# Optimization experiments

Measured on AMD Instinct MI355X. Metric: run time of the kernel, lower is better.

## Reference

```python
import jax, jax.numpy as jnp
import numpy as np
import math
jax.config.update("jax_enable_x64", True)

# dims matching init_kwargs
BS, N_IND, N_STEP, ORDER = 32, 8, 100, 2
N_ORD = ORDER + 1            # number of derivative orders tracked (y, y', y'')
N_IV, N_IV_STEPS = 2, 1
NVAR = N_STEP * N_ORD        # qp variables per ODE (eps column is dropped: A[..., 1:])
DT = jnp.float64             # solver_dbl=True


def _static_parts():
    # initial-value constraint rows: u[t, j] = iv_rhs for t < n_iv_steps, j < n_iv
    iv_rows = N_IV_STEPS * N_IV
    Iv = np.zeros((iv_rows, NVAR))
    r = 0
    for t in range(N_IV_STEPS):
        for j in range(N_IV):
            Iv[r, t * N_ORD + j] = 1.0
            r += 1
    # Taylor expansion tables: fact[i, j] = 1/(j-i)! for j>=i else 0; expn[i,j] = j-i
    i_idx = np.arange(ORDER)[:, None]
    j_idx = np.arange(N_ORD)[None, :]
    dmask = j_idx >= i_idx
    d = np.where(dmask, j_idx - i_idx, 0)
    fact = np.where(dmask, 1.0 / np.array([[math.factorial(v) for v in row] for row in d]), 0.0)
    sign = np.where(dmask, (-1.0) ** d, 0.0)
    Imat = np.eye(ORDER, N_ORD)
    return (jnp.asarray(Iv, DT), jnp.asarray(fact, DT), jnp.asarray(d, DT),
            jnp.asarray(sign, DT), jnp.asarray(Imat, DT))


def _solve(coeffs, rhs, iv_rhs, steps):
    # coeffs: (B, n_step, n_ord), rhs: (B, n_step), iv_rhs: (B, iv_rows), steps: (B, n_step-1)
    B = coeffs.shape[0]
    T1 = N_STEP - 1
    R = 2 * ORDER + 1  # fwd Taylor rows (ORDER) + bwd Taylor rows (ORDER) + central row (1)
    Iv, fact, expn, sign, Imat = _static_parts()

    # equation constraints: block-diagonal in step: sum_j coeffs[b,t,j] * u[t,j] = rhs[b,t]
    eye = jnp.eye(N_STEP, dtype=DT)
    Eq = jnp.einsum('ts,bsj->btsj', eye, coeffs).reshape(B, N_STEP, NVAR)
    IvB = jnp.broadcast_to(Iv[None], (B,) + Iv.shape)

    # smoothness constraints per interval t -> t+1 with step h = steps[b,t]
    h = steps[:, :, None, None]                  # (B, T1, 1, 1)
    hp = h ** expn                               # h^(j-i)
    fwd_t = fact * hp                            # fwd Taylor: sum_j h^(j-i)/(j-i)! u[t,j] - u[t+1,i] = 0
    bwd_t1 = fact * sign * hp                    # bwd Taylor: sum_j (-h)^(j-i)/(j-i)! u[t+1,j] - u[t,i] = 0
    ImB = jnp.broadcast_to(Imat, fwd_t.shape)
    hh = steps[:, :, None]                       # (B, T1, 1)
    e_m1 = jnp.zeros((N_ORD,), DT).at[ORDER - 1].set(1.0)
    e_o = jnp.zeros((N_ORD,), DT).at[ORDER].set(1.0)
    # central (trapezoid) rule on highest derivative:
    # u[t+1,ord-1] - u[t,ord-1] - h/2 (u[t,ord] + u[t+1,ord]) = 0
    ct = -e_m1 - 0.5 * hh * e_o                  # (B, T1, n_ord) coeffs on block t
    ct1 = e_m1 - 0.5 * hh * e_o                  # coeffs on block t+1
    Dt = jnp.concatenate([fwd_t, -ImB, ct[:, :, None, :]], axis=2)    # (B,T1,R,n_ord)
    Dt1 = jnp.concatenate([-ImB, bwd_t1, ct1[:, :, None, :]], axis=2)

    Dfull = jnp.zeros((B, T1, R, N_STEP, N_ORD), DT)
    t = jnp.arange(T1)
    Dfull = Dfull.at[:, t, :, t, :].set(jnp.moveaxis(Dt, 1, 0))
    Dfull = Dfull.at[:, t, :, t + 1, :].set(jnp.moveaxis(Dt1, 1, 0))
    D = Dfull.reshape(B, T1 * R, NVAR)

    A = jnp.concatenate([Eq, IvB, D], axis=1)    # dense AG (eps column dropped)
    beta = jnp.concatenate([rhs, iv_rhs, jnp.zeros((B, T1 * R), DT)], axis=1)

    AtA = jnp.einsum('bmi,bmj->bij', A, A)
    Atb = jnp.einsum('bmi,bm->bi', A, beta)
    L = jnp.linalg.cholesky(AtA)
    x = jax.scipy.linalg.cho_solve((L, True), Atb[..., None])[..., 0]
    return x


def setup_inputs() -> dict:
    key = jax.random.key(0)
    k1, k2, k3, k4 = jax.random.split(key, 4)
    coeffs = jax.random.normal(k1, (BS, N_IND, N_STEP, N_ORD), dtype=jnp.float32)
    rhs = jax.random.normal(k2, (BS, N_IND, N_STEP), dtype=jnp.float32)
    iv_rhs = jax.random.normal(k3, (BS, N_IND, N_IV_STEPS * N_IV), dtype=jnp.float32)
    # positive step sizes around the module's step_size=0.1
    steps = 0.05 + 0.1 * jax.random.uniform(k4, (BS, N_IND, N_STEP - 1), dtype=jnp.float32)
    return {"coeffs": coeffs, "rhs": rhs, "iv_rhs": iv_rhs, "steps": steps}


def reference(coeffs, rhs, iv_rhs, steps):
    B = BS * N_IND
    c = coeffs.reshape(B, N_STEP, N_ORD).astype(DT)   # n_dim = 1 folded in
    r = rhs.reshape(B, N_STEP).astype(DT)
    iv = iv_rhs.reshape(B, N_IV_STEPS * N_IV).astype(DT)
    st = steps.reshape(B, N_STEP - 1).astype(DT)
    x = _solve(c, r, iv, st)
    u = x.reshape(BS, N_IND, N_STEP, N_ORD)
    u0, u1, u2 = u[..., 0], u[..., 1], u[..., 2]
    eps = jnp.zeros((B,), DT)
    return (u0, u1, u2, eps, st[:, :, None])
```

## Files before the change

kernel.cpp:

```cpp
#include <hip/hip_runtime.h>

#define NPROB 256
#define NSTEP 100
#define T1    99

__device__ __forceinline__ void syminv3(const double A[6], double G[6]) {
    const double k00 = A[3] * A[5] - A[4] * A[4];
    const double k01 = A[2] * A[4] - A[1] * A[5];
    const double k02 = A[1] * A[4] - A[2] * A[3];
    const double det = A[0] * k00 + A[1] * k01 + A[2] * k02;
    const double id  = 1.0 / det;
    G[0] = k00 * id;
    G[1] = k01 * id;
    G[2] = k02 * id;
    G[3] = (A[0] * A[5] - A[2] * A[2]) * id;
    G[4] = (A[2] * A[1] - A[0] * A[4]) * id;
    G[5] = (A[0] * A[3] - A[1] * A[1]) * id;
}

__device__ __forceinline__ void symmul(const double G[6], const double M[9], double R[9]) {
#pragma unroll
    for (int c = 0; c < 3; ++c) {
        R[0 + c] = G[0] * M[c] + G[1] * M[3 + c] + G[2] * M[6 + c];
        R[3 + c] = G[1] * M[c] + G[3] * M[3 + c] + G[4] * M[6 + c];
        R[6 + c] = G[2] * M[c] + G[4] * M[3 + c] + G[5] * M[6 + c];
    }
}

__device__ __forceinline__ void symvec(const double G[6], const double v[3], double r[3]) {
    r[0] = G[0] * v[0] + G[1] * v[1] + G[2] * v[2];
    r[1] = G[1] * v[0] + G[3] * v[1] + G[4] * v[2];
    r[2] = G[2] * v[0] + G[4] * v[1] + G[5] * v[2];
}

__device__ __forceinline__ void pqz(const double A[6], const double C[9],
                                    const double B[9], const double b[3],
                                    double P[9], double Q[9], double z[3]) {
    double G[6];
    syminv3(A, G);
    symmul(G, C, P);
    symmul(G, B, Q);
    symvec(G, b, z);
}

__device__ __forceinline__ void store21(double* dst, const double P[9],
                                        const double Q[9], const double z[3]) {
#pragma unroll
    for (int k = 0; k < 9; ++k) { dst[k] = P[k]; dst[9 + k] = Q[k]; }
#pragma unroll
    for (int k = 0; k < 3; ++k) dst[18 + k] = z[k];
}

__device__ __forceinline__ void upd(double A[6], double C[9], double B[9], double b[3],
                                    const double* SL, const double* SR) {
    double Pl[9], Ql[9], zl[3], Pr[9], Qr[9], zr[3];
#pragma unroll
    for (int k = 0; k < 9; ++k) { Pl[k] = SL[k]; Ql[k] = SL[9 + k]; }
#pragma unroll
    for (int k = 0; k < 3; ++k) zl[k] = SL[18 + k];
#pragma unroll
    for (int k = 0; k < 9; ++k) { Pr[k] = SR[k]; Qr[k] = SR[9 + k]; }
#pragma unroll
    for (int k = 0; k < 3; ++k) zr[k] = SR[18 + k];

    const int RI[6] = {0, 0, 0, 1, 1, 2};
    const int CI[6] = {0, 1, 2, 1, 2, 2};
#pragma unroll
    for (int e = 0; e < 6; ++e) {
        const int r = RI[e], c = CI[e];
        A[e] -= C[3 * r] * Ql[c] + C[3 * r + 1] * Ql[3 + c] + C[3 * r + 2] * Ql[6 + c]
              + B[3 * r] * Pr[c] + B[3 * r + 1] * Pr[3 + c] + B[3 * r + 2] * Pr[6 + c];
    }
    double nC[9], nB[9];
#pragma unroll
    for (int r = 0; r < 3; ++r)
#pragma unroll
        for (int c = 0; c < 3; ++c) {
            nC[3 * r + c] = -(C[3 * r] * Pl[c] + C[3 * r + 1] * Pl[3 + c] + C[3 * r + 2] * Pl[6 + c]);
            nB[3 * r + c] = -(B[3 * r] * Qr[c] + B[3 * r + 1] * Qr[3 + c] + B[3 * r + 2] * Qr[6 + c]);
        }
#pragma unroll
    for (int r = 0; r < 3; ++r)
        b[r] -= C[3 * r] * zl[0] + C[3 * r + 1] * zl[1] + C[3 * r + 2] * zl[2]
              + B[3 * r] * zr[0] + B[3 * r + 1] * zr[1] + B[3 * r + 2] * zr[2];
#pragma unroll
    for (int k = 0; k < 9; ++k) { C[k] = nC[k]; B[k] = nB[k]; }
}

__device__ __forceinline__ void build_row(int t, const float* cb, const float* rb,
                                          const float* sb, const float* ivp,
                                          double A[6], double C[9], double B[9], double b[3]) {
    const double c0 = (double)cb[t * 3 + 0];
    const double c1 = (double)cb[t * 3 + 1];
    const double c2 = (double)cb[t * 3 + 2];
    const double r  = (double)rb[t];
    A[0] = c0 * c0; A[1] = c0 * c1; A[2] = c0 * c2;
    A[3] = c1 * c1; A[4] = c1 * c2; A[5] = c2 * c2;
    b[0] = c0 * r;  b[1] = c1 * r;  b[2] = c2 * r;
#pragma unroll
    for (int k = 0; k < 9; ++k) { C[k] = 0.0; B[k] = 0.0; }

    if (t == 0) {
        A[0] += 1.0; A[3] += 1.0;
        b[0] += (double)ivp[0];
        b[1] += (double)ivp[1];
    }
    if (t < T1) {
        const double h = (double)sb[t], h2 = h * h;
        A[0] += 2.0;
        A[1] += h;
        A[2] += 0.5 * h2;
        A[3] += h2 + 3.0;
        A[4] += 0.5 * h2 * h + 1.5 * h;
        A[5] += 0.25 * h2 * h2 + 1.25 * h2;
        B[0] = -2.0;       B[1] =  h;         B[2] = -0.5 * h2;
        B[3] = -h;         B[4] = -3.0;       B[5] =  1.5 * h;
        B[6] = -0.5 * h2;  B[7] = -1.5 * h;   B[8] =  0.25 * h2;
    }
    if (t > 0) {
        const double hm = (double)sb[t - 1], hm2 = hm * hm;
        A[0] += 2.0;
        A[1] -= hm;
        A[2] += 0.5 * hm2;
        A[3] += hm2 + 3.0;
        A[4] -= 0.5 * hm2 * hm + 1.5 * hm;
        A[5] += 0.25 * hm2 * hm2 + 1.25 * hm2;
        C[0] = -2.0;       C[1] = -hm;        C[2] = -0.5 * hm2;
        C[3] =  hm;        C[4] = -3.0;       C[5] = -1.5 * hm;
        C[6] = -0.5 * hm2; C[7] =  1.5 * hm;  C[8] =  0.25 * hm2;
    }
}

__global__ __launch_bounds__(64, 1) void ode_pcr_kernel(
    const float* __restrict__ coeffs,
    const float* __restrict__ rhs,
    const float* __restrict__ iv_rhs,
    const float* __restrict__ steps,
    float* __restrict__ out)
{
    const int b = blockIdx.x;
    const int L = threadIdx.x;

    __shared__ double S[114][21];
    __shared__ double X[52][3];

    for (int i = L; i < 114 * 21; i += 64) ((double*)S)[i] = 0.0;
    for (int i = L; i < 52 * 3;  i += 64) ((double*)X)[i] = 0.0;

    const float* cb  = coeffs + b * NSTEP * 3;
    const float* rb  = rhs    + b * NSTEP;
    const float* sb  = steps  + b * T1;
    const float* ivp = iv_rhs + b * 2;

    const bool act = (L < 50);
    double Ae[6], Ce[9], Be[9], be[3];
    double Po[9], Qo[9], zo[3];

    __syncthreads();

    if (act) {
        build_row(2 * L, cb, rb, sb, ivp, Ae, Ce, Be, be);
        double Ao[6], Co[9], Bo[9], bo[3];
        build_row(2 * L + 1, cb, rb, sb, ivp, Ao, Co, Bo, bo);
        pqz(Ao, Co, Bo, bo, Po, Qo, zo);
        store21(&S[L + 32][0], Po, Qo, zo);
    }
    __syncthreads();
    if (act) upd(Ae, Ce, Be, be, &S[L + 31][0], &S[L + 32][0]);
    __syncthreads();

#pragma unroll
    for (int lv = 0; lv < 6; ++lv) {
        const int s = 1 << lv;
        if (act) {
            double P[9], Q[9], z[3];
            pqz(Ae, Ce, Be, be, P, Q, z);
            store21(&S[L + 32][0], P, Q, z);
        }
        __syncthreads();
        if (act) upd(Ae, Ce, Be, be, &S[L + 32 - s][0], &S[L + 32 + s][0]);
        __syncthreads();
    }

    double xe[3] = {0.0, 0.0, 0.0};
    if (act) {
        double G[6];
        syminv3(Ae, G);
        symvec(G, be, xe);
        X[L + 1][0] = xe[0]; X[L + 1][1] = xe[1]; X[L + 1][2] = xe[2];
    }
    __syncthreads();

    if (act) {
        const double xr0 = X[L + 2][0], xr1 = X[L + 2][1], xr2 = X[L + 2][2];
        double xo[3];
#pragma unroll
        for (int r = 0; r < 3; ++r)
            xo[r] = zo[r]
                  - (Po[3 * r] * xe[0] + Po[3 * r + 1] * xe[1] + Po[3 * r + 2] * xe[2])
                  - (Qo[3 * r] * xr0   + Qo[3 * r + 1] * xr1   + Qo[3 * r + 2] * xr2);

        const int t0 = 2 * L, t1 = 2 * L + 1;
        out[            b * NSTEP + t0] = (float)xe[0];
        out[            b * NSTEP + t1] = (float)xo[0];
        out[25600 +     b * NSTEP + t0] = (float)xe[1];
        out[25600 +     b * NSTEP + t1] = (float)xo[1];
        out[51200 +     b * NSTEP + t0] = (float)xe[2];
        out[51200 +     b * NSTEP + t1] = (float)xo[2];
    }

    for (int t = L; t < T1; t += 64)
        out[77056 + b * T1 + t] = sb[t];
    if (L == 0)
        out[76800 + b] = 0.0f;
}

extern "C" void kernel_launch(void* const* d_in, const int* in_sizes, int n_in,
                              void* d_out, int out_size, void* d_ws, size_t ws_size,
                              hipStream_t stream) {
    const float* coeffs = (const float*)d_in[0];
    const float* rhs    = (const float*)d_in[1];
    const float* iv_rhs = (const float*)d_in[2];
    const float* steps  = (const float*)d_in[3];
    float* out = (float*)d_out;

    ode_pcr_kernel<<<dim3(NPROB), dim3(64), 0, stream>>>(
        coeffs, rhs, iv_rhs, steps, out);
}
```

Baseline: 66.89 us.

## Switch PCR solver to fp32 and exchange neighbor blocks via wavefront shuffles

```diff
diff --git a/kernel.cpp b/kernel.cpp
--- a/kernel.cpp
+++ b/kernel.cpp
@@ -4,12 +4,12 @@
 #define NSTEP 100
 #define T1    99
 
-__device__ __forceinline__ void syminv3(const double A[6], double G[6]) {
-    const double k00 = A[3] * A[5] - A[4] * A[4];
-    const double k01 = A[2] * A[4] - A[1] * A[5];
-    const double k02 = A[1] * A[4] - A[2] * A[3];
-    const double det = A[0] * k00 + A[1] * k01 + A[2] * k02;
-    const double id  = 1.0 / det;
+__device__ __forceinline__ void syminv3(const float A[6], float G[6]) {
+    const float k00 = A[3] * A[5] - A[4] * A[4];
+    const float k01 = A[2] * A[4] - A[1] * A[5];
+    const float k02 = A[1] * A[4] - A[2] * A[3];
+    const float det = A[0] * k00 + A[1] * k01 + A[2] * k02;
+    const float id  = 1.0f / det;
     G[0] = k00 * id;
     G[1] = k01 * id;
     G[2] = k02 * id;
@@ -18,7 +18,7 @@
     G[5] = (A[0] * A[3] - A[1] * A[1]) * id;
 }
 
-__device__ __forceinline__ void symmul(const double G[6], const double M[9], double R[9]) {
+__device__ __forceinline__ void symmul(const float G[6], const float M[9], float R[9]) {
 #pragma unroll
     for (int c = 0; c < 3; ++c) {
         R[0 + c] = G[0] * M[c] + G[1] * M[3 + c] + G[2] * M[6 + c];
@@ -27,41 +27,25 @@
     }
 }
 
-__device__ __forceinline__ void symvec(const double G[6], const double v[3], double r[3]) {
+__device__ __forceinline__ void symvec(const float G[6], const float v[3], float r[3]) {
     r[0] = G[0] * v[0] + G[1] * v[1] + G[2] * v[2];
     r[1] = G[1] * v[0] + G[3] * v[1] + G[4] * v[2];
     r[2] = G[2] * v[0] + G[4] * v[1] + G[5] * v[2];
 }
 
-__device__ __forceinline__ void pqz(const double A[6], const double C[9],
-                                    const double B[9], const double b[3],
-                                    double P[9], double Q[9], double z[3]) {
-    double G[6];
+__device__ __forceinline__ void pqz(const float A[6], const float C[9],
+                                    const float B[9], const float b[3], float pub[21]) {
+    float G[6];
     syminv3(A, G);
-    symmul(G, C, P);
-    symmul(G, B, Q);
-    symvec(G, b, z);
-}
-
-__device__ __forceinline__ void store21(double* dst, const double P[9],
-                                        const double Q[9], const double z[3]) {
-#pragma unroll
-    for (int k = 0; k < 9; ++k) { dst[k] = P[k]; dst[9 + k] = Q[k]; }
-#pragma unroll
-    for (int k = 0; k < 3; ++k) dst[18 + k] = z[k];
-}
-
-__device__ __forceinline__ void upd(double A[6], double C[9], double B[9], double b[3],
-                                    const double* SL, const double* SR) {
-    double Pl[9], Ql[9], zl[3], Pr[9], Qr[9], zr[3];
-#pragma unroll
-    for (int k = 0; k < 9; ++k) { Pl[k] = SL[k]; Ql[k] = SL[9 + k]; }
-#pragma unroll
-    for (int k = 0; k < 3; ++k) zl[k] = SL[18 + k];
-#pragma unroll
-    for (int k = 0; k < 9; ++k) { Pr[k] = SR[k]; Qr[k] = SR[9 + k]; }
-#pragma unroll
-    for (int k = 0; k < 3; ++k) zr[k] = SR[18 + k];
+    symmul(G, C, pub);
+    symmul(G, B, pub + 9);
+    symvec(G, b, pub + 18);
+}
+
+__device__ __forceinline__ void upd(float A[6], float C[9], float B[9], float b[3],
+                                    const float SL[21], const float SR[21]) {
+    const float* Pl = SL;      const float* Ql = SL + 9;  const float* zl = SL + 18;
+    const float* Pr = SR;      const float* Qr = SR + 9;  const float* zr = SR + 18;
 
     const int RI[6] = {0, 0, 0, 1, 1, 2};
     const int CI[6] = {0, 1, 2, 1, 2, 2};
@@ -71,7 +55,7 @@
         A[e] -= C[3 * r] * Ql[c] + C[3 * r + 1] * Ql[3 + c] + C[3 * r + 2] * Ql[6 + c]
               + B[3 * r] * Pr[c] + B[3 * r + 1] * Pr[3 + c] + B[3 * r + 2] * Pr[6 + c];
     }
-    double nC[9], nB[9];
+    float nC[9], nB[9];
 #pragma unroll
     for (int r = 0; r < 3; ++r)
 #pragma unroll
@@ -89,49 +73,58 @@
 
 __device__ __forceinline__ void build_row(int t, const float* cb, const float* rb,
                                           const float* sb, const float* ivp,
-                                          double A[6], double C[9], double B[9], double b[3]) {
-    const double c0 = (double)cb[t * 3 + 0];
-    const double c1 = (double)cb[t * 3 + 1];
-    const double c2 = (double)cb[t * 3 + 2];
-    const double r  = (double)rb[t];
+                                          float A[6], float C[9], float B[9], float b[3]) {
+    const float c0 = cb[t * 3 + 0];
+    const float c1 = cb[t * 3 + 1];
+    const float c2 = cb[t * 3 + 2];
+    const float r  = rb[t];
     A[0] = c0 * c0; A[1] = c0 * c1; A[2] = c0 * c2;
     A[3] = c1 * c1; A[4] = c1 * c2; A[5] = c2 * c2;
     b[0] = c0 * r;  b[1] = c1 * r;  b[2] = c2 * r;
 #pragma unroll
-    for (int k = 0; k < 9; ++k) { C[k] = 0.0; B[k] = 0.0; }
+    for (int k = 0; k < 9; ++k) { C[k] = 0.0f; B[k] = 0.0f; }
 
     if (t == 0) {
-        A[0] += 1.0; A[3] += 1.0;
-        b[0] += (double)ivp[0];
-        b[1] += (double)ivp[1];
+        A[0] += 1.0f; A[3] += 1.0f;
+        b[0] += ivp[0];
+        b[1] += ivp[1];
     }
     if (t < T1) {
-        const double h = (double)sb[t], h2 = h * h;
-        A[0] += 2.0;
+        const float h = sb[t], h2 = h * h;
+        A[0] += 2.0f;
         A[1] += h;
-        A[2] += 0.5 * h2;
-        A[3] += h2 + 3.0;
-        A[4] += 0.5 * h2 * h + 1.5 * h;
-        A[5] += 0.25 * h2 * h2 + 1.25 * h2;
-        B[0] = -2.0;       B[1] =  h;         B[2] = -0.5 * h2;
-        B[3] = -h;         B[4] = -3.0;       B[5] =  1.5 * h;
-        B[6] = -0.5 * h2;  B[7] = -1.5 * h;   B[8] =  0.25 * h2;
+        A[2] += 0.5f * h2;
+        A[3] += h2 + 3.0f;
+        A[4] += 0.5f * h2 * h + 1.5f * h;
+        A[5] += 0.25f * h2 * h2 + 1.25f * h2;
+        B[0] = -2.0f;      B[1] =  h;        B[2] = -0.5f * h2;
+        B[3] = -h;         B[4] = -3.0f;     B[5] =  1.5f * h;
+        B[6] = -0.5f * h2; B[7] = -1.5f * h; B[8] =  0.25f * h2;
     }
     if (t > 0) {
-        const double hm = (double)sb[t - 1], hm2 = hm * hm;
-        A[0] += 2.0;
+        const float hm = sb[t - 1], hm2 = hm * hm;
+        A[0] += 2.0f;
         A[1] -= hm;
-        A[2] += 0.5 * hm2;
-        A[3] += hm2 + 3.0;
-        A[4] -= 0.5 * hm2 * hm + 1.5 * hm;
-        A[5] += 0.25 * hm2 * hm2 + 1.25 * hm2;
-        C[0] = -2.0;       C[1] = -hm;        C[2] = -0.5 * hm2;
-        C[3] =  hm;        C[4] = -3.0;       C[5] = -1.5 * hm;
-        C[6] = -0.5 * hm2; C[7] =  1.5 * hm;  C[8] =  0.25 * hm2;
-    }
-}
-
-__global__ __launch_bounds__(64, 1) void ode_pcr_kernel(
+        A[2] += 0.5f * hm2;
+        A[3] += hm2 + 3.0f;
+        A[4] -= 0.5f * hm2 * hm + 1.5f * hm;
+        A[5] += 0.25f * hm2 * hm2 + 1.25f * hm2;
+        C[0] = -2.0f;      C[1] = -hm;       C[2] = -0.5f * hm2;
+        C[3] =  hm;        C[4] = -3.0f;     C[5] = -1.5f * hm;
+        C[6] = -0.5f * hm2; C[7] = 1.5f * hm; C[8] = 0.25f * hm2;
+    }
+}
+
+__device__ __forceinline__ void shflup21(const float v[21], float o[21], int s) {
+#pragma unroll
+    for (int k = 0; k < 21; ++k) o[k] = __shfl_up(v[k], s, 64);
+}
+__device__ __forceinline__ void shfldn21(const float v[21], float o[21], int s) {
+#pragma unroll
+    for (int k = 0; k < 21; ++k) o[k] = __shfl_down(v[k], s, 64);
+}
+
+__global__ __launch_bounds__(64, 1) void ode_pcr_shfl_kernel(
     const float* __restrict__ coeffs,
     const float* __restrict__ rhs,
     const float* __restrict__ iv_rhs,
@@ -140,73 +133,77 @@
 {
     const int b = blockIdx.x;
     const int L = threadIdx.x;
-
-    __shared__ double S[114][21];
-    __shared__ double X[52][3];
-
-    for (int i = L; i < 114 * 21; i += 64) ((double*)S)[i] = 0.0;
-    for (int i = L; i < 52 * 3;  i += 64) ((double*)X)[i] = 0.0;
+    const bool act = (L < 50);
 
     const float* cb  = coeffs + b * NSTEP * 3;
     const float* rb  = rhs    + b * NSTEP;
     const float* sb  = steps  + b * T1;
     const float* ivp = iv_rhs + b * 2;
 
-    const bool act = (L < 50);
-    double Ae[6], Ce[9], Be[9], be[3];
-    double Po[9], Qo[9], zo[3];
-
-    __syncthreads();
+    float Ae[6], Ce[9], Be[9], be[3];
+    float pubo[21];
+#pragma unroll
+    for (int k = 0; k < 21; ++k) pubo[k] = 0.0f;
+#pragma unroll
+    for (int k = 0; k < 6; ++k) Ae[k] = 0.0f;
+#pragma unroll
+    for (int k = 0; k < 9; ++k) { Ce[k] = 0.0f; Be[k] = 0.0f; }
+    be[0] = be[1] = be[2] = 0.0f;
 
     if (act) {
         build_row(2 * L, cb, rb, sb, ivp, Ae, Ce, Be, be);
-        double Ao[6], Co[9], Bo[9], bo[3];
+        float Ao[6], Co[9], Bo[9], bo[3];
         build_row(2 * L + 1, cb, rb, sb, ivp, Ao, Co, Bo, bo);
-        pqz(Ao, Co, Bo, bo, Po, Qo, zo);
-        store21(&S[L + 32][0], Po, Qo, zo);
-    }
-    __syncthreads();
-    if (act) upd(Ae, Ce, Be, be, &S[L + 31][0], &S[L + 32][0]);
-    __syncthreads();
+        pqz(Ao, Co, Bo, bo, pubo);
+    }
+    {
+        float SL[21];
+        shflup21(pubo, SL, 1);
+        if (act) upd(Ae, Ce, Be, be, SL, pubo);
+    }
 
 #pragma unroll
     for (int lv = 0; lv < 6; ++lv) {
         const int s = 1 << lv;
-        if (act) {
-            double P[9], Q[9], z[3];
-            pqz(Ae, Ce, Be, be, P, Q, z);
-            store21(&S[L + 32][0], P, Q, z);
-        }
-        __syncthreads();
-        if (act) upd(Ae, Ce, Be, be, &S[L + 32 - s][0], &S[L + 32 + s][0]);
-        __syncthreads();
-    }
-
-    double xe[3] = {0.0, 0.0, 0.0};
+        float pub[21];
+#pragma unroll
+        for (int k = 0; k < 21; ++k) pub[k] = 0.0f;
+        if (act) pqz(Ae, Ce, Be, be, pub);
+        float SL[21], SR[21];
+        shflup21(pub, SL, s);
+        shfldn21(pub, SR, s);
+        if (act) upd(Ae, Ce, Be, be, SL, SR);
+    }
+
+    float xe[3] = {0.0f, 0.0f, 0.0f};
     if (act) {
-        double G[6];
+        float G[6];
         syminv3(Ae, G);
         symvec(G, be, xe);
-        X[L + 1][0] = xe[0]; X[L + 1][1] = xe[1]; X[L + 1][2] = xe[2];
-    }
-    __syncthreads();
+    }
+    float xr[3];
+    xr[0] = __shfl_down(xe[0], 1, 64);
+    xr[1] = __shfl_down(xe[1], 1, 64);
+    xr[2] = __shfl_down(xe[2], 1, 64);
 
     if (act) {
-        const double xr0 = X[L + 2][0], xr1 = X[L + 2][1], xr2 = X[L + 2][2];
-        double xo[3];
+        const float* Po = pubo;
+        const float* Qo = pubo + 9;
+        const float* zo = pubo + 18;
+        float xo[3];
 #pragma unroll
         for (int r = 0; r < 3; ++r)
             xo[r] = zo[r]
                   - (Po[3 * r] * xe[0] + Po[3 * r + 1] * xe[1] + Po[3 * r + 2] * xe[2])
-                  - (Qo[3 * r] * xr0   + Qo[3 * r + 1] * xr1   + Qo[3 * r + 2] * xr2);
+                  - (Qo[3 * r] * xr[0] + Qo[3 * r + 1] * xr[1] + Qo[3 * r + 2] * xr[2]);
 
         const int t0 = 2 * L, t1 = 2 * L + 1;
-        out[            b * NSTEP + t0] = (float)xe[0];
-        out[            b * NSTEP + t1] = (float)xo[0];
-        out[25600 +     b * NSTEP + t0] = (float)xe[1];
-        out[25600 +     b * NSTEP + t1] = (float)xo[1];
-        out[51200 +     b * NSTEP + t0] = (float)xe[2];
-        out[51200 +     b * NSTEP + t1] = (float)xo[2];
+        out[            b * NSTEP + t0] = xe[0];
+        out[            b * NSTEP + t1] = xo[0];
+        out[25600 +     b * NSTEP + t0] = xe[1];
+        out[25600 +     b * NSTEP + t1] = xo[1];
+        out[51200 +     b * NSTEP + t0] = xe[2];
+        out[51200 +     b * NSTEP + t1] = xo[2];
     }
 
     for (int t = L; t < T1; t += 64)
@@ -224,6 +221,6 @@
     const float* steps  = (const float*)d_in[3];
     float* out = (float*)d_out;
 
-    ode_pcr_kernel<<<dim3(NPROB), dim3(64), 0, stream>>>(
+    ode_pcr_shfl_kernel<<<dim3(NPROB), dim3(64), 0, stream>>>(
         coeffs, rhs, iv_rhs, steps, out);
 }
```

New measurement: 65.13 us. 1.03x faster.
